# Kernel optimization log

Measured on AMD Instinct MI355X. Metric: run time of the kernel, lower is better.

Reference implementation:

```python
import jax, jax.numpy as jnp
import numpy as np

MARGIN = 1.0
EPS = 1e-8


def setup_inputs() -> dict:
    key = jax.random.key(0)
    k1, k2 = jax.random.split(key)
    B, D, NUM_CLASSES = 8192, 512, 100
    features = jax.random.normal(k1, (B, D), dtype=jnp.float32)
    labels = jax.random.randint(k2, (B,), 0, NUM_CLASSES, dtype=jnp.int64)
    return {"features": features, "labels": labels}


def _metric_tensor(features):
    # G = I + feature covariance (curvature-aware metric on the feature manifold)
    B, D = features.shape
    centered = features - jnp.mean(features, axis=0, keepdims=True)
    cov = jnp.einsum('bi,bj->ij', centered, centered) / jnp.float32(B)
    return jnp.eye(D, dtype=features.dtype) + cov


def _masked_random_idx(mask, key):
    # gumbel-max trick: uniform random index among True entries of each row of mask [B,B]
    g = -jnp.log(-jnp.log(jax.random.uniform(key, mask.shape, dtype=jnp.float32) + EPS) + EPS)
    scores = jnp.where(mask, g, -jnp.inf)
    return jnp.argmax(scores, axis=1)


def reference(features, labels):
    B = features.shape[0]
    G = _metric_tensor(features)

    same = labels[:, None] == labels[None, :]              # [B,B]
    not_self = ~jnp.eye(B, dtype=bool)
    pos_mask = same & not_self
    neg_mask = ~same

    kp, kn = jax.random.split(jax.random.key(42))
    pos_idx = _masked_random_idx(pos_mask, kp)             # [B]
    neg_idx = _masked_random_idx(neg_mask, kn)             # [B]
    valid = jnp.any(pos_mask, axis=1) & jnp.any(neg_mask, axis=1)

    diff_p = features - features[pos_idx]                  # [B,D]
    diff_n = features - features[neg_idx]                  # [B,D]
    # Riemannian distance: sqrt((x-y)^T G (x-y))
    d_pos = jnp.sqrt(jnp.einsum('bi,ij,bj->b', diff_p, G, diff_p) + EPS)
    d_neg = jnp.sqrt(jnp.einsum('bi,ij,bj->b', diff_n, G, diff_n) + EPS)

    per_sample = jnp.maximum(d_pos - d_neg + MARGIN, 0.0)
    per_sample = jnp.where(valid, per_sample, 0.0)
    n_valid = jnp.maximum(jnp.sum(valid.astype(jnp.float32)), 1.0)
    return jnp.sum(per_sample) / n_valid
```

## Files before the change

kernel.cpp:

```cpp
#include <hip/hip_runtime.h>
#include <stdint.h>

#define BSZ   8192
#define DIM   512

typedef __attribute__((ext_vector_type(8))) short short8;
typedef __attribute__((ext_vector_type(4))) float f32x4;
typedef __attribute__((ext_vector_type(8))) uint16_t u16x8;

__host__ __device__ inline uint16_t f2bf(float x) {
  uint32_t u = __float_as_uint(x);
  return (uint16_t)((u + 0x7FFFu + ((u >> 16) & 1u)) >> 16);
}
__host__ __device__ inline float bf2f(uint16_t h) {
  return __uint_as_float(((uint32_t)h) << 16);
}

__host__ __device__ inline uint32_t rotl32(uint32_t v, int s) {
#if defined(__HIP_DEVICE_COMPILE__) && __has_builtin(__builtin_amdgcn_alignbit)
  return __builtin_amdgcn_alignbit(v, v, 32 - s);
#else
  return (v << s) | (v >> (32 - s));
#endif
}

__host__ __device__ inline void threefry2x32(uint32_t k0, uint32_t k1,
                                             uint32_t x0, uint32_t x1,
                                             uint32_t& o0, uint32_t& o1) {
  uint32_t ks2 = k0 ^ k1 ^ 0x1BD11BDAu;
  x0 += k0; x1 += k1;
  x0 += x1; x1 = rotl32(x1, 13); x1 ^= x0;
  x0 += x1; x1 = rotl32(x1, 15); x1 ^= x0;
  x0 += x1; x1 = rotl32(x1, 26); x1 ^= x0;
  x0 += x1; x1 = rotl32(x1,  6); x1 ^= x0;
  x0 += k1; x1 += ks2 + 1u;
  x0 += x1; x1 = rotl32(x1, 17); x1 ^= x0;
  x0 += x1; x1 = rotl32(x1, 29); x1 ^= x0;
  x0 += x1; x1 = rotl32(x1, 16); x1 ^= x0;
  x0 += x1; x1 = rotl32(x1, 24); x1 ^= x0;
  x0 += ks2; x1 += k0 + 2u;
  x0 += x1; x1 = rotl32(x1, 13); x1 ^= x0;
  x0 += x1; x1 = rotl32(x1, 15); x1 ^= x0;
  x0 += x1; x1 = rotl32(x1, 26); x1 ^= x0;
  x0 += x1; x1 = rotl32(x1,  6); x1 ^= x0;
  x0 += k0; x1 += k1 + 3u;
  x0 += x1; x1 = rotl32(x1, 17); x1 ^= x0;
  x0 += x1; x1 = rotl32(x1, 29); x1 ^= x0;
  x0 += x1; x1 = rotl32(x1, 16); x1 ^= x0;
  x0 += x1; x1 = rotl32(x1, 24); x1 ^= x0;
  x0 += k1; x1 += ks2 + 4u;
  x0 += x1; x1 = rotl32(x1, 13); x1 ^= x0;
  x0 += x1; x1 = rotl32(x1, 15); x1 ^= x0;
  x0 += x1; x1 = rotl32(x1, 26); x1 ^= x0;
  x0 += x1; x1 = rotl32(x1,  6); x1 ^= x0;
  x0 += ks2; x1 += k0 + 5u;
  o0 = x0; o1 = x1;
}

constexpr size_t OFF_CTR    = 0;
constexpr size_t OFF_S      = 1024;
constexpr size_t OFF_BSTART = 3072;
constexpr size_t OFF_BIDX   = 4096;
constexpr size_t OFF_PIDX   = 36864;
constexpr size_t OFF_NIDX   = 69632;
constexpr size_t OFF_LPART  = 102400;
constexpr size_t OFF_GB     = 131072;
constexpr size_t OFF_FB     = 2097152;
constexpr size_t OFF_HB     = 10485760;
constexpr size_t ZERO_BYTES = 3072;

__global__ __launch_bounds__(256) void prep_kernel(const float* __restrict__ F,
                                                   uint16_t* __restrict__ Fb,
                                                   float* __restrict__ S) {
  int i = (blockIdx.x * 256 + threadIdx.x) * 8;
  float4 a = *(const float4*)&F[i];
  float4 b = *(const float4*)&F[i + 4];
  u16x8 o;
  o[0] = f2bf(a.x); o[1] = f2bf(a.y); o[2] = f2bf(a.z); o[3] = f2bf(a.w);
  o[4] = f2bf(b.x); o[5] = f2bf(b.y); o[6] = f2bf(b.z); o[7] = f2bf(b.w);
  *(u16x8*)&Fb[i] = o;
  if (blockIdx.x < 256) {
    int b0 = blockIdx.x * 32;
    int t = threadIdx.x;
    float s0 = 0.f, s1 = 0.f;
    for (int r = 0; r < 32; ++r) {
      const float* row = F + (size_t)(b0 + r) * DIM;
      s0 += row[t];
      s1 += row[t + 256];
    }
    atomicAdd(&S[t], s0);
    atomicAdd(&S[t + 256], s1);
  }
}

__global__ __launch_bounds__(256) void covmat_mfma_kernel(const uint16_t* __restrict__ Fb,
                                                          float* __restrict__ Mpart) {
  __shared__ uint16_t sA[64][40];
  __shared__ uint16_t sB[64][40];
  int i0 = blockIdx.x * 64;
  int j0 = blockIdx.y * 64;
  int kc0 = blockIdx.z * 2048;
  int tid = threadIdx.x;
  int lane = tid & 63, wid = tid >> 6, quad = lane >> 4, l16 = lane & 15;
  int wm = (wid >> 1) * 32;
  int wn = (wid & 1) * 32;
  int sk = tid & 31;
  int sm = (tid >> 5) * 8;
  f32x4 acc[2][2] = {};
  for (int kk = 0; kk < 2048; kk += 32) {
    int krow = kc0 + kk + sk;
    u16x8 va = *(const u16x8*)&Fb[(size_t)krow * DIM + i0 + sm];
    u16x8 vb = *(const u16x8*)&Fb[(size_t)krow * DIM + j0 + sm];
    __syncthreads();
#pragma unroll
    for (int jj = 0; jj < 8; ++jj) { sA[sm + jj][sk] = va[jj]; sB[sm + jj][sk] = vb[jj]; }
    __syncthreads();
#pragma unroll
    for (int r = 0; r < 2; ++r) {
      short8 af = *(short8*)&sA[wm + r * 16 + l16][quad * 8];
#pragma unroll
      for (int c = 0; c < 2; ++c) {
        short8 bf = *(short8*)&sB[wn + c * 16 + l16][quad * 8];
        acc[r][c] = __builtin_amdgcn_mfma_f32_16x16x32_bf16(af, bf, acc[r][c], 0, 0, 0);
      }
    }
  }
  float* out = Mpart + (size_t)blockIdx.z * DIM * DIM;
#pragma unroll
  for (int r = 0; r < 2; ++r)
#pragma unroll
    for (int c = 0; c < 2; ++c)
#pragma unroll
      for (int g = 0; g < 4; ++g)
        out[(size_t)(i0 + wm + r * 16 + quad * 4 + g) * DIM + j0 + wn + c * 16 + l16] = acc[r][c][g];
}

__global__ __launch_bounds__(256) void buildG_kernel(const float* __restrict__ Mpart,
                                                     const float* __restrict__ S,
                                                     uint16_t* __restrict__ Gb) {
  int idx = blockIdx.x * 256 + threadIdx.x;
  int i = idx >> 9, j = idx & 511;
  float m = Mpart[idx] + Mpart[(size_t)DIM * DIM + idx] +
            Mpart[2 * (size_t)DIM * DIM + idx] + Mpart[3 * (size_t)DIM * DIM + idx];
  const float invB = 1.0f / (float)BSZ;
  float mi = S[i] * invB, mj = S[j] * invB;
  Gb[idx] = f2bf(m * invB - mi * mj + (i == j ? 1.0f : 0.0f));
}

__global__ __launch_bounds__(256) void bucket_kernel(const int* __restrict__ labels,
                                                     int* __restrict__ bucketStart,
                                                     int* __restrict__ bucketIdx) {
  __shared__ int cnt[128];
  __shared__ int base[128];
  int tid = threadIdx.x;
  if (tid < 128) cnt[tid] = 0;
  __syncthreads();
  for (int b = tid; b < BSZ; b += 256) atomicAdd(&cnt[labels[b]], 1);
  __syncthreads();
  if (tid == 0) {
    int run = 0;
    for (int c = 0; c < 100; ++c) { base[c] = run; bucketStart[c] = run; run += cnt[c]; }
    bucketStart[100] = run;
  }
  __syncthreads();
  for (int b = tid; b < BSZ; b += 256) {
    int p = atomicAdd(&base[labels[b]], 1);
    bucketIdx[p] = b;
  }
}

struct SharedMM  { uint16_t sA[128][72]; uint16_t sB[64][72]; };
struct SharedNeg { uint8_t slab[BSZ]; unsigned long long wmax[4]; int curRow; };
union __align__(16) SharedU { SharedMM mm; SharedNeg neg; };

__global__ __launch_bounds__(256) void overlap_kernel(
    const uint16_t* __restrict__ Fb, const uint16_t* __restrict__ Gb,
    uint16_t* __restrict__ Hb, const int* __restrict__ labels,
    const int* __restrict__ bStart, const int* __restrict__ bIdx,
    int* __restrict__ posIdx, int* __restrict__ negIdx,
    int* __restrict__ rowCtr,
    uint32_t kp0, uint32_t kp1, uint32_t kn0, uint32_t kn1) {
  __shared__ SharedU sh;
  int bid = blockIdx.x, tid = threadIdx.x;
  int lane = tid & 63, wid = tid >> 6, quad = lane >> 4, l16 = lane & 15;

  if (bid < 224) {
    int am = tid & 127, ah = (tid >> 7) * 32;
    int bk = tid >> 2, bn = (tid & 3) * 16;
    int tm = wid * 32;
    for (int t = bid; t < 512; t += 224) {
      int n0 = (t & 7) * 64;
      int m0 = (t >> 3) * 128;
      f32x4 acc[2][4] = {};
      for (int k0 = 0; k0 < DIM; k0 += 64) {
        {
          const uint16_t* src = &Fb[(size_t)(m0 + am) * DIM + k0 + ah];
#pragma unroll
          for (int v = 0; v < 4; ++v)
            *(u16x8*)&sh.mm.sA[am][ah + v * 8] = *(const u16x8*)&src[v * 8];
        }
        {
          u16x8 g0 = *(const u16x8*)&Gb[(size_t)(k0 + bk) * DIM + n0 + bn];
          u16x8 g1 = *(const u16x8*)&Gb[(size_t)(k0 + bk) * DIM + n0 + bn + 8];
#pragma unroll
          for (int jj = 0; jj < 8; ++jj) { sh.mm.sB[bn + jj][bk] = g0[jj]; sh.mm.sB[bn + 8 + jj][bk] = g1[jj]; }
        }
        __syncthreads();
#pragma unroll
        for (int k32 = 0; k32 < 64; k32 += 32) {
          short8 af[2];
#pragma unroll
          for (int r = 0; r < 2; ++r)
            af[r] = *(short8*)&sh.mm.sA[tm + r * 16 + l16][k32 + quad * 8];
#pragma unroll
          for (int c = 0; c < 4; ++c) {
            short8 bf = *(short8*)&sh.mm.sB[c * 16 + l16][k32 + quad * 8];
#pragma unroll
            for (int r = 0; r < 2; ++r)
              acc[r][c] = __builtin_amdgcn_mfma_f32_16x16x32_bf16(af[r], bf, acc[r][c], 0, 0, 0);
          }
        }
        __syncthreads();
      }
#pragma unroll
      for (int r = 0; r < 2; ++r)
#pragma unroll
        for (int c = 0; c < 4; ++c)
#pragma unroll
          for (int g = 0; g < 4; ++g)
            Hb[(size_t)(m0 + tm + r * 16 + quad * 4 + g) * DIM + n0 + c * 16 + l16] = f2bf(acc[r][c][g]);
    }
    __syncthreads();
  } else if (bid < 256) {
    for (int row = (bid - 224) * 4 + wid; row < BSZ; row += 128) {
      int cls = labels[row];
      int s = bStart[cls], e = bStart[cls + 1];
      uint32_t base = (uint32_t)(row << 13);
      unsigned long long best = 0;
      for (int t2 = s + lane; t2 < e; t2 += 64) {
        int cc = bIdx[t2];
        uint32_t a0, a1;
        threefry2x32(kp0, kp1, 0u, base + (uint32_t)cc, a0, a1);
        unsigned long long comp = ((unsigned long long)((a0 ^ a1) >> 9) << 32) | (uint32_t)(~cc);
        if (cc == row) comp = 0;
        if (comp > best) best = comp;
      }
#pragma unroll
      for (int off = 32; off; off >>= 1) {
        unsigned long long o = __shfl_down(best, off);
        if (o > best) best = o;
      }
      if (lane == 0) posIdx[row] = best ? (int)(~(uint32_t)best) : -1;
    }
    __syncthreads();
  }

  {
    uint32_t* s32 = (uint32_t*)sh.neg.slab;
#pragma unroll
    for (int pass = 0; pass < 8; ++pass) {
      int idx = pass * 1024 + tid * 4;
      int4 l4 = *(const int4*)&labels[idx];
      uint32_t packed = (uint32_t)(l4.x & 0xFF) | ((uint32_t)(l4.y & 0xFF) << 8) |
                        ((uint32_t)(l4.z & 0xFF) << 16) | ((uint32_t)(l4.w & 0xFF) << 24);
      s32[pass * 256 + tid] = packed;
    }
  }
  __syncthreads();
  while (true) {
    if (tid == 0) sh.neg.curRow = atomicAdd(rowCtr, 1);
    __syncthreads();
    int row = sh.neg.curRow;
    if (row >= BSZ) break;
    uint32_t li = sh.neg.slab[row];
    uint32_t base = (uint32_t)(row << 13);
    unsigned long long bA = 0, bB = 0, bC = 0, bD = 0;
#pragma unroll 2
    for (int it = 0; it < 8; ++it) {
      int c0 = tid + (it << 10);
      int c1 = c0 + 256, c2 = c0 + 512, c3 = c0 + 768;
      uint32_t l0 = sh.neg.slab[c0], l1 = sh.neg.slab[c1], l2 = sh.neg.slab[c2], l3 = sh.neg.slab[c3];
      uint32_t a0, a1, e0, e1, f0, f1, g0, g1;
      threefry2x32(kn0, kn1, 0u, base + (uint32_t)c0, a0, a1);
      threefry2x32(kn0, kn1, 0u, base + (uint32_t)c1, e0, e1);
      threefry2x32(kn0, kn1, 0u, base + (uint32_t)c2, f0, f1);
      threefry2x32(kn0, kn1, 0u, base + (uint32_t)c3, g0, g1);
      unsigned long long compA = ((unsigned long long)((a0 ^ a1) >> 9) << 32) | (uint32_t)(~c0);
      unsigned long long compB = ((unsigned long long)((e0 ^ e1) >> 9) << 32) | (uint32_t)(~c1);
      unsigned long long compC = ((unsigned long long)((f0 ^ f1) >> 9) << 32) | (uint32_t)(~c2);
      unsigned long long compD = ((unsigned long long)((g0 ^ g1) >> 9) << 32) | (uint32_t)(~c3);
      if (l0 == li) compA = 0;
      if (l1 == li) compB = 0;
      if (l2 == li) compC = 0;
      if (l3 == li) compD = 0;
      if (compA > bA) bA = compA;
      if (compB > bB) bB = compB;
      if (compC > bC) bC = compC;
      if (compD > bD) bD = compD;
    }
    if (bB > bA) bA = bB;
    if (bC > bA) bA = bC;
    if (bD > bA) bA = bD;
    unsigned long long best = bA;
#pragma unroll
    for (int off = 32; off; off >>= 1) {
      unsigned long long o = __shfl_down(best, off);
      if (o > best) best = o;
    }
    if (lane == 0) sh.neg.wmax[wid] = best;
    __syncthreads();
    if (tid == 0) {
      best = sh.neg.wmax[0];
      for (int w = 1; w < 4; ++w) if (sh.neg.wmax[w] > best) best = sh.neg.wmax[w];
      negIdx[row] = best ? (int)(~(uint32_t)best) : -1;
    }
    __syncthreads();
  }
}

__global__ __launch_bounds__(256) void loss_kernel(const float* __restrict__ F,
                                                   const uint16_t* __restrict__ Hb,
                                                   const int* __restrict__ posIdx,
                                                   const int* __restrict__ negIdx,
                                                   float2* __restrict__ lossPart) {
  __shared__ float2 part[4];
  int row = blockIdx.x * 4 + (threadIdx.x >> 6);
  int lane = threadIdx.x & 63;
  int p = posIdx[row], n = negIdx[row];
  bool valid = (p >= 0) && (n >= 0);
  int ps = valid ? p : row;
  int ns = valid ? n : row;
  int k = lane * 8;
  const float* Fi = F + (size_t)row * DIM + k;
  const float* Fp = F + (size_t)ps * DIM + k;
  const float* Fn = F + (size_t)ns * DIM + k;
  u16x8 h_i = *(const u16x8*)(Hb + (size_t)row * DIM + k);
  u16x8 h_p = *(const u16x8*)(Hb + (size_t)ps * DIM + k);
  u16x8 h_n = *(const u16x8*)(Hb + (size_t)ns * DIM + k);
  float4 fi0 = *(const float4*)&Fi[0], fi1 = *(const float4*)&Fi[4];
  float4 fp0 = *(const float4*)&Fp[0], fp1 = *(const float4*)&Fp[4];
  float4 fn0 = *(const float4*)&Fn[0], fn1 = *(const float4*)&Fn[4];
  float fi[8] = {fi0.x, fi0.y, fi0.z, fi0.w, fi1.x, fi1.y, fi1.z, fi1.w};
  float fp[8] = {fp0.x, fp0.y, fp0.z, fp0.w, fp1.x, fp1.y, fp1.z, fp1.w};
  float fn[8] = {fn0.x, fn0.y, fn0.z, fn0.w, fn1.x, fn1.y, fn1.z, fn1.w};
  float qii = 0.f, qpp = 0.f, qip = 0.f, qnn = 0.f, qin = 0.f;
#pragma unroll
  for (int jj = 0; jj < 8; ++jj) {
    float hi = bf2f(h_i[jj]), hp = bf2f(h_p[jj]), hn = bf2f(h_n[jj]);
    qii += fi[jj] * hi;
    qpp += fp[jj] * hp;
    qip += fi[jj] * hp;
    qnn += fn[jj] * hn;
    qin += fi[jj] * hn;
  }
#pragma unroll
  for (int off = 32; off > 0; off >>= 1) {
    qii += __shfl_down(qii, off);
    qpp += __shfl_down(qpp, off);
    qip += __shfl_down(qip, off);
    qnn += __shfl_down(qnn, off);
    qin += __shfl_down(qin, off);
  }
  if (lane == 0) {
    float d2p = fmaxf(qii + qpp - 2.f * qip, 0.f);
    float d2n = fmaxf(qii + qnn - 2.f * qin, 0.f);
    float v = fmaxf(sqrtf(d2p + 1e-8f) - sqrtf(d2n + 1e-8f) + 1.0f, 0.0f);
    if (!valid) v = 0.f;
    part[threadIdx.x >> 6] = make_float2(v, valid ? 1.f : 0.f);
  }
  __syncthreads();
  if (threadIdx.x == 0) {
    float s = 0.f, c = 0.f;
#pragma unroll
    for (int w = 0; w < 4; ++w) { s += part[w].x; c += part[w].y; }
    lossPart[blockIdx.x] = make_float2(s, c);
  }
}

__global__ __launch_bounds__(256) void finalize_kernel(const float2* __restrict__ lossPart,
                                                       float* __restrict__ out) {
  __shared__ float2 wsum[4];
  int tid = threadIdx.x;
  float s = 0.f, c = 0.f;
  for (int z = tid; z < 2048; z += 256) {
    float2 v = lossPart[z];
    s += v.x; c += v.y;
  }
#pragma unroll
  for (int off = 32; off > 0; off >>= 1) {
    s += __shfl_down(s, off);
    c += __shfl_down(c, off);
  }
  if ((tid & 63) == 0) wsum[tid >> 6] = make_float2(s, c);
  __syncthreads();
  if (tid == 0) {
    s = 0.f; c = 0.f;
#pragma unroll
    for (int w = 0; w < 4; ++w) { s += wsum[w].x; c += wsum[w].y; }
    out[0] = s / fmaxf(c, 1.0f);
  }
}

extern "C" void kernel_launch(void* const* d_in, const int* in_sizes, int n_in,
                              void* d_out, int out_size, void* d_ws, size_t ws_size,
                              hipStream_t stream) {
  const float* F = (const float*)d_in[0];
  const int* labels = (const int*)d_in[1];
  float* out = (float*)d_out;
  char* ws = (char*)d_ws;

  int* rowCtr    = (int*)(ws + OFF_CTR);
  float* S       = (float*)(ws + OFF_S);
  int* bStart    = (int*)(ws + OFF_BSTART);
  int* bIdx      = (int*)(ws + OFF_BIDX);
  int* posIdx    = (int*)(ws + OFF_PIDX);
  int* negIdx    = (int*)(ws + OFF_NIDX);
  float2* lPart  = (float2*)(ws + OFF_LPART);
  uint16_t* Gb   = (uint16_t*)(ws + OFF_GB);
  uint16_t* Fb   = (uint16_t*)(ws + OFF_FB);
  uint16_t* Hb   = (uint16_t*)(ws + OFF_HB);
  float* Mpart   = (float*)(ws + OFF_HB);

  uint32_t kp0, kp1, kn0, kn1;
  threefry2x32(0u, 42u, 0u, 0u, kp0, kp1);
  threefry2x32(0u, 42u, 0u, 1u, kn0, kn1);

  hipMemsetAsync(ws, 0, ZERO_BYTES, stream);

  prep_kernel<<<2048, 256, 0, stream>>>(F, Fb, S);

  dim3 covGrid(8, 8, 4);
  covmat_mfma_kernel<<<covGrid, 256, 0, stream>>>(Fb, Mpart);

  buildG_kernel<<<(DIM * DIM) / 256, 256, 0, stream>>>(Mpart, S, Gb);

  bucket_kernel<<<1, 256, 0, stream>>>(labels, bStart, bIdx);

  overlap_kernel<<<1024, 256, 0, stream>>>(Fb, Gb, Hb, labels, bStart, bIdx,
                                           posIdx, negIdx, rowCtr,
                                           kp0, kp1, kn0, kn1);

  loss_kernel<<<BSZ / 4, 256, 0, stream>>>(F, Hb, posIdx, negIdx, lPart);

  finalize_kernel<<<1, 256, 0, stream>>>(lPart, out);
}
```

Before: 332.1 us.

## Exploit covariance symmetry, fuse bucketing into covmat, fuse finalize via last-block reduction

The covariance kernel computes only upper-triangular 64x64 tiles (36 of 64 per k-chunk), and buildG mirrors the lower triangle from them. The bucket kernel becomes an extra block of the covariance launch, and the finalize kernel is folded into the loss kernel through an atomic done-counter last-block reduction. The loss kernel also reads the bf16 copy of the features instead of fp32. These changes remove two launches and some redundant matmul work. The cost is slightly lower precision in the loss and a counter that relies on the existing workspace memset to be zeroed.

```diff
diff --git a/kernel.cpp b/kernel.cpp
--- a/kernel.cpp
+++ b/kernel.cpp
@@ -58,6 +58,7 @@
 }
 
 constexpr size_t OFF_CTR    = 0;
+constexpr size_t OFF_DONE   = 4;
 constexpr size_t OFF_S      = 1024;
 constexpr size_t OFF_BSTART = 3072;
 constexpr size_t OFF_BIDX   = 4096;
@@ -93,46 +94,71 @@
   }
 }
 
-__global__ __launch_bounds__(256) void covmat_mfma_kernel(const uint16_t* __restrict__ Fb,
-                                                          float* __restrict__ Mpart) {
-  __shared__ uint16_t sA[64][40];
-  __shared__ uint16_t sB[64][40];
-  int i0 = blockIdx.x * 64;
-  int j0 = blockIdx.y * 64;
-  int kc0 = blockIdx.z * 2048;
-  int tid = threadIdx.x;
-  int lane = tid & 63, wid = tid >> 6, quad = lane >> 4, l16 = lane & 15;
-  int wm = (wid >> 1) * 32;
-  int wn = (wid & 1) * 32;
-  int sk = tid & 31;
-  int sm = (tid >> 5) * 8;
-  f32x4 acc[2][2] = {};
-  for (int kk = 0; kk < 2048; kk += 32) {
-    int krow = kc0 + kk + sk;
-    u16x8 va = *(const u16x8*)&Fb[(size_t)krow * DIM + i0 + sm];
-    u16x8 vb = *(const u16x8*)&Fb[(size_t)krow * DIM + j0 + sm];
-    __syncthreads();
-#pragma unroll
-    for (int jj = 0; jj < 8; ++jj) { sA[sm + jj][sk] = va[jj]; sB[sm + jj][sk] = vb[jj]; }
-    __syncthreads();
-#pragma unroll
-    for (int r = 0; r < 2; ++r) {
-      short8 af = *(short8*)&sA[wm + r * 16 + l16][quad * 8];
-#pragma unroll
-      for (int c = 0; c < 2; ++c) {
-        short8 bf = *(short8*)&sB[wn + c * 16 + l16][quad * 8];
-        acc[r][c] = __builtin_amdgcn_mfma_f32_16x16x32_bf16(af, bf, acc[r][c], 0, 0, 0);
+union CovShared {
+  struct { uint16_t sA[64][40]; uint16_t sB[64][40]; } mm;
+  struct { int cnt[128]; int base[128]; } bk;
+};
+
+__global__ __launch_bounds__(256) void covmat_bucket_kernel(
+    const uint16_t* __restrict__ Fb, float* __restrict__ Mpart,
+    const int* __restrict__ labels, int* __restrict__ bucketStart,
+    int* __restrict__ bucketIdx) {
+  __shared__ CovShared sh;
+  int bid = blockIdx.x, tid = threadIdx.x;
+  if (bid < 144) {
+    int chunk = bid & 3;
+    int t = bid >> 2;
+    int rem = t, ti = 0;
+    while (rem >= 8 - ti) { rem -= 8 - ti; ++ti; }
+    int tj = ti + rem;
+    int i0 = ti * 64, j0 = tj * 64;
+    int kc0 = chunk * 2048;
+    int lane = tid & 63, wid = tid >> 6, quad = lane >> 4, l16 = lane & 15;
+    int wm = (wid >> 1) * 32, wn = (wid & 1) * 32;
+    int sk = tid & 31, sm = (tid >> 5) * 8;
+    f32x4 acc[2][2] = {};
+    for (int kk = 0; kk < 2048; kk += 32) {
+      int krow = kc0 + kk + sk;
+      u16x8 va = *(const u16x8*)&Fb[(size_t)krow * DIM + i0 + sm];
+      u16x8 vb = *(const u16x8*)&Fb[(size_t)krow * DIM + j0 + sm];
+      __syncthreads();
+#pragma unroll
+      for (int jj = 0; jj < 8; ++jj) { sh.mm.sA[sm + jj][sk] = va[jj]; sh.mm.sB[sm + jj][sk] = vb[jj]; }
+      __syncthreads();
+#pragma unroll
+      for (int r = 0; r < 2; ++r) {
+        short8 af = *(short8*)&sh.mm.sA[wm + r * 16 + l16][quad * 8];
+#pragma unroll
+        for (int c = 0; c < 2; ++c) {
+          short8 bf = *(short8*)&sh.mm.sB[wn + c * 16 + l16][quad * 8];
+          acc[r][c] = __builtin_amdgcn_mfma_f32_16x16x32_bf16(af, bf, acc[r][c], 0, 0, 0);
+        }
       }
     }
-  }
-  float* out = Mpart + (size_t)blockIdx.z * DIM * DIM;
-#pragma unroll
-  for (int r = 0; r < 2; ++r)
-#pragma unroll
-    for (int c = 0; c < 2; ++c)
-#pragma unroll
-      for (int g = 0; g < 4; ++g)
-        out[(size_t)(i0 + wm + r * 16 + quad * 4 + g) * DIM + j0 + wn + c * 16 + l16] = acc[r][c][g];
+    float* outp = Mpart + (size_t)chunk * DIM * DIM;
+#pragma unroll
+    for (int r = 0; r < 2; ++r)
+#pragma unroll
+      for (int c = 0; c < 2; ++c)
+#pragma unroll
+        for (int g = 0; g < 4; ++g)
+          outp[(size_t)(i0 + wm + r * 16 + quad * 4 + g) * DIM + j0 + wn + c * 16 + l16] = acc[r][c][g];
+  } else {
+    if (tid < 128) sh.bk.cnt[tid] = 0;
+    __syncthreads();
+    for (int b = tid; b < BSZ; b += 256) atomicAdd(&sh.bk.cnt[labels[b]], 1);
+    __syncthreads();
+    if (tid == 0) {
+      int run = 0;
+      for (int c = 0; c < 100; ++c) { sh.bk.base[c] = run; bucketStart[c] = run; run += sh.bk.cnt[c]; }
+      bucketStart[100] = run;
+    }
+    __syncthreads();
+    for (int b = tid; b < BSZ; b += 256) {
+      int p = atomicAdd(&sh.bk.base[labels[b]], 1);
+      bucketIdx[p] = b;
+    }
+  }
 }
 
 __global__ __launch_bounds__(256) void buildG_kernel(const float* __restrict__ Mpart,
@@ -140,33 +166,14 @@
                                                      uint16_t* __restrict__ Gb) {
   int idx = blockIdx.x * 256 + threadIdx.x;
   int i = idx >> 9, j = idx & 511;
-  float m = Mpart[idx] + Mpart[(size_t)DIM * DIM + idx] +
-            Mpart[2 * (size_t)DIM * DIM + idx] + Mpart[3 * (size_t)DIM * DIM + idx];
+  int a = i < j ? i : j;
+  int b = i < j ? j : i;
+  size_t sidx = (size_t)a * DIM + b;
+  float m = Mpart[sidx] + Mpart[(size_t)DIM * DIM + sidx] +
+            Mpart[2 * (size_t)DIM * DIM + sidx] + Mpart[3 * (size_t)DIM * DIM + sidx];
   const float invB = 1.0f / (float)BSZ;
   float mi = S[i] * invB, mj = S[j] * invB;
   Gb[idx] = f2bf(m * invB - mi * mj + (i == j ? 1.0f : 0.0f));
-}
-
-__global__ __launch_bounds__(256) void bucket_kernel(const int* __restrict__ labels,
-                                                     int* __restrict__ bucketStart,
-                                                     int* __restrict__ bucketIdx) {
-  __shared__ int cnt[128];
-  __shared__ int base[128];
-  int tid = threadIdx.x;
-  if (tid < 128) cnt[tid] = 0;
-  __syncthreads();
-  for (int b = tid; b < BSZ; b += 256) atomicAdd(&cnt[labels[b]], 1);
-  __syncthreads();
-  if (tid == 0) {
-    int run = 0;
-    for (int c = 0; c < 100; ++c) { base[c] = run; bucketStart[c] = run; run += cnt[c]; }
-    bucketStart[100] = run;
-  }
-  __syncthreads();
-  for (int b = tid; b < BSZ; b += 256) {
-    int p = atomicAdd(&base[labels[b]], 1);
-    bucketIdx[p] = b;
-  }
 }
 
 struct SharedMM  { uint16_t sA[128][72]; uint16_t sB[64][72]; };
@@ -318,12 +325,13 @@
   }
 }
 
-__global__ __launch_bounds__(256) void loss_kernel(const float* __restrict__ F,
-                                                   const uint16_t* __restrict__ Hb,
-                                                   const int* __restrict__ posIdx,
-                                                   const int* __restrict__ negIdx,
-                                                   float2* __restrict__ lossPart) {
+__global__ __launch_bounds__(256) void loss_final_kernel(
+    const uint16_t* __restrict__ Fb, const uint16_t* __restrict__ Hb,
+    const int* __restrict__ posIdx, const int* __restrict__ negIdx,
+    float2* __restrict__ lossPart, int* __restrict__ doneCtr,
+    float* __restrict__ out) {
   __shared__ float2 part[4];
+  __shared__ bool isLast;
   int row = blockIdx.x * 4 + (threadIdx.x >> 6);
   int lane = threadIdx.x & 63;
   int p = posIdx[row], n = negIdx[row];
@@ -331,27 +339,22 @@
   int ps = valid ? p : row;
   int ns = valid ? n : row;
   int k = lane * 8;
-  const float* Fi = F + (size_t)row * DIM + k;
-  const float* Fp = F + (size_t)ps * DIM + k;
-  const float* Fn = F + (size_t)ns * DIM + k;
+  u16x8 f_i = *(const u16x8*)(Fb + (size_t)row * DIM + k);
+  u16x8 f_p = *(const u16x8*)(Fb + (size_t)ps * DIM + k);
+  u16x8 f_n = *(const u16x8*)(Fb + (size_t)ns * DIM + k);
   u16x8 h_i = *(const u16x8*)(Hb + (size_t)row * DIM + k);
   u16x8 h_p = *(const u16x8*)(Hb + (size_t)ps * DIM + k);
   u16x8 h_n = *(const u16x8*)(Hb + (size_t)ns * DIM + k);
-  float4 fi0 = *(const float4*)&Fi[0], fi1 = *(const float4*)&Fi[4];
-  float4 fp0 = *(const float4*)&Fp[0], fp1 = *(const float4*)&Fp[4];
-  float4 fn0 = *(const float4*)&Fn[0], fn1 = *(const float4*)&Fn[4];
-  float fi[8] = {fi0.x, fi0.y, fi0.z, fi0.w, fi1.x, fi1.y, fi1.z, fi1.w};
-  float fp[8] = {fp0.x, fp0.y, fp0.z, fp0.w, fp1.x, fp1.y, fp1.z, fp1.w};
-  float fn[8] = {fn0.x, fn0.y, fn0.z, fn0.w, fn1.x, fn1.y, fn1.z, fn1.w};
   float qii = 0.f, qpp = 0.f, qip = 0.f, qnn = 0.f, qin = 0.f;
 #pragma unroll
   for (int jj = 0; jj < 8; ++jj) {
+    float fi = bf2f(f_i[jj]), fp = bf2f(f_p[jj]), fn = bf2f(f_n[jj]);
     float hi = bf2f(h_i[jj]), hp = bf2f(h_p[jj]), hn = bf2f(h_n[jj]);
-    qii += fi[jj] * hi;
-    qpp += fp[jj] * hp;
-    qip += fi[jj] * hp;
-    qnn += fn[jj] * hn;
-    qin += fi[jj] * hn;
+    qii += fi * hi;
+    qpp += fp * hp;
+    qip += fi * hp;
+    qnn += fn * hn;
+    qin += fi * hn;
   }
 #pragma unroll
   for (int off = 32; off > 0; off >>= 1) {
@@ -374,30 +377,31 @@
 #pragma unroll
     for (int w = 0; w < 4; ++w) { s += part[w].x; c += part[w].y; }
     lossPart[blockIdx.x] = make_float2(s, c);
-  }
-}
-
-__global__ __launch_bounds__(256) void finalize_kernel(const float2* __restrict__ lossPart,
-                                                       float* __restrict__ out) {
-  __shared__ float2 wsum[4];
-  int tid = threadIdx.x;
-  float s = 0.f, c = 0.f;
-  for (int z = tid; z < 2048; z += 256) {
-    float2 v = lossPart[z];
-    s += v.x; c += v.y;
-  }
-#pragma unroll
-  for (int off = 32; off > 0; off >>= 1) {
-    s += __shfl_down(s, off);
-    c += __shfl_down(c, off);
-  }
-  if ((tid & 63) == 0) wsum[tid >> 6] = make_float2(s, c);
+    __threadfence();
+    isLast = (atomicAdd(doneCtr, 1) == 2047);
+  }
   __syncthreads();
-  if (tid == 0) {
-    s = 0.f; c = 0.f;
-#pragma unroll
-    for (int w = 0; w < 4; ++w) { s += wsum[w].x; c += wsum[w].y; }
-    out[0] = s / fmaxf(c, 1.0f);
+  if (isLast) {
+    __threadfence();
+    int tid = threadIdx.x;
+    float s = 0.f, c = 0.f;
+    for (int z = tid; z < 2048; z += 256) {
+      float2 v = lossPart[z];
+      s += v.x; c += v.y;
+    }
+#pragma unroll
+    for (int off = 32; off > 0; off >>= 1) {
+      s += __shfl_down(s, off);
+      c += __shfl_down(c, off);
+    }
+    if (lane == 0) part[tid >> 6] = make_float2(s, c);
+    __syncthreads();
+    if (tid == 0) {
+      s = 0.f; c = 0.f;
+#pragma unroll
+      for (int w = 0; w < 4; ++w) { s += part[w].x; c += part[w].y; }
+      out[0] = s / fmaxf(c, 1.0f);
+    }
   }
 }
 
@@ -410,6 +414,7 @@
   char* ws = (char*)d_ws;
 
   int* rowCtr    = (int*)(ws + OFF_CTR);
+  int* doneCtr   = (int*)(ws + OFF_DONE);
   float* S       = (float*)(ws + OFF_S);
   int* bStart    = (int*)(ws + OFF_BSTART);
   int* bIdx      = (int*)(ws + OFF_BIDX);
@@ -429,18 +434,14 @@
 
   prep_kernel<<<2048, 256, 0, stream>>>(F, Fb, S);
 
-  dim3 covGrid(8, 8, 4);
-  covmat_mfma_kernel<<<covGrid, 256, 0, stream>>>(Fb, Mpart);
+  covmat_bucket_kernel<<<145, 256, 0, stream>>>(Fb, Mpart, labels, bStart, bIdx);
 
   buildG_kernel<<<(DIM * DIM) / 256, 256, 0, stream>>>(Mpart, S, Gb);
-
-  bucket_kernel<<<1, 256, 0, stream>>>(labels, bStart, bIdx);
 
   overlap_kernel<<<1024, 256, 0, stream>>>(Fb, Gb, Hb, labels, bStart, bIdx,
                                            posIdx, negIdx, rowCtr,
                                            kp0, kp1, kn0, kn1);
 
-  loss_kernel<<<BSZ / 4, 256, 0, stream>>>(F, Hb, posIdx, negIdx, lPart);
-
-  finalize_kernel<<<1, 256, 0, stream>>>(lPart, out);
-}
+  loss_final_kernel<<<BSZ / 4, 256, 0, stream>>>(Fb, Hb, posIdx, negIdx,
+                                                 lPart, doneCtr, out);
+}
```

Measured after the change: 370.2 us. 11.5% more time.
